# Kernel tuning notes

Hardware: AMD Instinct MI355X
Metric: run time of the kernel (lower is better)

The kernel has to match this reference:

```python
import jax, jax.numpy as jnp
import numpy as np

EPS = 1e-10       # module eps
COS_EPS = 1e-8    # torch F.cosine_similarity norm clamp
TAO = 0.0
LIP = 0.0
SQUARED = False
DETACH_HR = True
LAMB_LIP = 1
# p = 1.0 -> np.random.random() < p is always True, so the sampling mask is baked to True.


def setup_inputs() -> dict:
    key = jax.random.key(0)
    k1, k2, k3 = jax.random.split(key, 3)
    img = jax.random.normal(k1, (256, 4, 3, 112, 112), dtype=jnp.float32)
    feat = jax.random.normal(k2, (256, 4, 512), dtype=jnp.float32)
    feat_norm = jax.random.normal(k3, (256, 4, 1), dtype=jnp.float32)
    return {"img": img, "feat": feat, "feat_norm": feat_norm}


def reference(img, feat, feat_norm):
    # img: [B, K, C, H, W], feat: [B, K, D], feat_norm: [B, K, 1]
    fn0 = feat_norm[:, 0, 0]                                   # [B]
    cond = fn0 > -TAO                                          # [B] outer if per batch row
    w = jax.lax.stop_gradient(1.0 / (jnp.exp(fn0) + EPS))      # [B] adaptive weight (detached)

    # consecutive-frame image L2 distance (full-tensor sum per frame pair)
    img_diff = jnp.sqrt(jnp.sum((img[:, 1:] - img[:, :-1]) ** 2, axis=(2, 3, 4))) + EPS  # [B, K-1]
    # skip frames identical to frame 0 (torch.equal check)
    neq = jnp.any(img[:, 1:] != img[:, 0:1], axis=(2, 3, 4))   # [B, K-1]

    fa = feat[:, :-1]                                          # [B, K-1, D] (HR side of each pair)
    fb = feat[:, 1:]                                           # [B, K-1, D]
    if DETACH_HR:
        fa = jax.lax.stop_gradient(fa)
    na = jnp.maximum(jnp.linalg.norm(fa, axis=-1), COS_EPS)
    nb = jnp.maximum(jnp.linalg.norm(fb, axis=-1), COS_EPS)
    cos = jnp.sum(fa * fb, axis=-1) / (na * nb)                # [B, K-1]

    ratio = (1.0 - cos) / img_diff - LIP
    term = ratio ** 2 if SQUARED else jnp.maximum(ratio, 0.0)
    term = term * w[:, None]

    mask = cond[:, None] & neq
    penalty = jnp.sum(jnp.where(mask, term, 0.0), axis=1)      # [B]
    adaptive_weight_list = jnp.where(cond, w, 0.0)             # [B]
    return LAMB_LIP * jnp.mean(penalty), adaptive_weight_list
```

## Files before the change

### kernel.cpp

```cpp
#include <hip/hip_runtime.h>
#include <math.h>

#define EPS 1e-10f
#define COS_EPS 1e-8f

#define NB 256
#define NF 4
#define FRAME_F4 9408
#define BLK_PER_B 37
#define PART_STRIDE 64


__global__ __launch_bounds__(256) void img_stage(const float* __restrict__ img,
                                                 float* __restrict__ ws_sq_part,
                                                 int* __restrict__ ws_neq_part) {
    const int b   = blockIdx.y;
    const int bx  = blockIdx.x;
    const int tid = threadIdx.x;
    const int idx = bx * 256 + tid;

    float s1 = 0.f, s2 = 0.f, s3 = 0.f;
    int   n1 = 0,   n2 = 0,   n3 = 0;

    if (idx < FRAME_F4) {
        const float4* base = (const float4*)img + (size_t)b * NF * FRAME_F4;
        float4 f0 = base[idx];
        float4 f1 = base[FRAME_F4 + idx];
        float4 f2 = base[2 * FRAME_F4 + idx];
        float4 f3 = base[3 * FRAME_F4 + idx];

        float dx, dy, dz, dw;
        dx = f1.x - f0.x; dy = f1.y - f0.y; dz = f1.z - f0.z; dw = f1.w - f0.w;
        s1 = dx*dx + dy*dy + dz*dz + dw*dw;
        dx = f2.x - f1.x; dy = f2.y - f1.y; dz = f2.z - f1.z; dw = f2.w - f1.w;
        s2 = dx*dx + dy*dy + dz*dz + dw*dw;
        dx = f3.x - f2.x; dy = f3.y - f2.y; dz = f3.z - f2.z; dw = f3.w - f2.w;
        s3 = dx*dx + dy*dy + dz*dz + dw*dw;

        n1 = (f1.x != f0.x) | (f1.y != f0.y) | (f1.z != f0.z) | (f1.w != f0.w);
        n2 = (f2.x != f0.x) | (f2.y != f0.y) | (f2.z != f0.z) | (f2.w != f0.w);
        n3 = (f3.x != f0.x) | (f3.y != f0.y) | (f3.z != f0.z) | (f3.w != f0.w);
    }

    for (int off = 32; off > 0; off >>= 1) {
        s1 += __shfl_down(s1, off);
        s2 += __shfl_down(s2, off);
        s3 += __shfl_down(s3, off);
        n1 |= __shfl_down(n1, off);
        n2 |= __shfl_down(n2, off);
        n3 |= __shfl_down(n3, off);
    }

    __shared__ float ls[3][4];
    __shared__ int   ln[3][4];
    const int wave = tid >> 6;
    if ((tid & 63) == 0) {
        ls[0][wave] = s1; ls[1][wave] = s2; ls[2][wave] = s3;
        ln[0][wave] = n1; ln[1][wave] = n2; ln[2][wave] = n3;
    }
    __syncthreads();
    if (tid == 0) {
        const int base3 = b * 3;
        ws_sq_part[(base3 + 0) * PART_STRIDE + bx] = ls[0][0] + ls[0][1] + ls[0][2] + ls[0][3];
        ws_sq_part[(base3 + 1) * PART_STRIDE + bx] = ls[1][0] + ls[1][1] + ls[1][2] + ls[1][3];
        ws_sq_part[(base3 + 2) * PART_STRIDE + bx] = ls[2][0] + ls[2][1] + ls[2][2] + ls[2][3];
        ws_neq_part[(base3 + 0) * PART_STRIDE + bx] = ln[0][0] | ln[0][1] | ln[0][2] | ln[0][3];
        ws_neq_part[(base3 + 1) * PART_STRIDE + bx] = ln[1][0] | ln[1][1] | ln[1][2] | ln[1][3];
        ws_neq_part[(base3 + 2) * PART_STRIDE + bx] = ln[2][0] | ln[2][1] | ln[2][2] | ln[2][3];
    }
}

__global__ __launch_bounds__(192) void batch_stage(const float* __restrict__ feat,
                                                   const float* __restrict__ feat_norm,
                                                   const float* __restrict__ ws_sq_part,
                                                   const int* __restrict__ ws_neq_part,
                                                   float* __restrict__ out) {
    const int b    = blockIdx.x;
    const int tid  = threadIdx.x;
    const int p    = tid >> 6;
    const int lane = tid & 63;

    const float4* fa = (const float4*)feat + ((size_t)b * NF + p) * 128;
    const float4* fb = fa + 128;

    float dab = 0.f, daa = 0.f, dbb = 0.f;
#pragma unroll
    for (int j = 0; j < 2; ++j) {
        float4 a  = fa[lane + 64 * j];
        float4 bb = fb[lane + 64 * j];
        dab += a.x * bb.x + a.y * bb.y + a.z * bb.z + a.w * bb.w;
        daa += a.x * a.x + a.y * a.y + a.z * a.z + a.w * a.w;
        dbb += bb.x * bb.x + bb.y * bb.y + bb.z * bb.z + bb.w * bb.w;
    }

    const int slot = (b * 3 + p) * PART_STRIDE + lane;
    float sq = (lane < BLK_PER_B) ? ws_sq_part[slot] : 0.0f;
    int   nq = (lane < BLK_PER_B) ? ws_neq_part[slot] : 0;

    for (int off = 32; off > 0; off >>= 1) {
        dab += __shfl_down(dab, off);
        daa += __shfl_down(daa, off);
        dbb += __shfl_down(dbb, off);
        sq  += __shfl_down(sq, off);
        nq  |= __shfl_down(nq, off);
    }

    __shared__ float sh_term[3];
    if (lane == 0) {
        float na   = fmaxf(sqrtf(daa), COS_EPS);
        float nb   = fmaxf(sqrtf(dbb), COS_EPS);
        float cosv = dab / (na * nb);
        float img_diff = sqrtf(sq) + EPS;
        float ratio = (1.0f - cosv) / img_diff;
        float term  = fmaxf(ratio, 0.0f);
        float fn0   = feat_norm[b * NF];
        float w     = 1.0f / (expf(fn0) + EPS);
        bool  cond  = fn0 > 0.0f;
        sh_term[p]  = (cond && nq) ? term * w : 0.0f;
    }
    __syncthreads();
    if (tid == 0) {
        float fn0 = feat_norm[b * NF];
        float w   = 1.0f / (expf(fn0) + EPS);
        out[1 + b] = (fn0 > 0.0f) ? w : 0.0f;
        float pen = sh_term[0] + sh_term[1] + sh_term[2];
        atomicAdd(&out[0], pen * (1.0f / 256.0f));
    }
}

extern "C" void kernel_launch(void* const* d_in, const int* in_sizes, int n_in,
                              void* d_out, int out_size, void* d_ws, size_t ws_size,
                              hipStream_t stream) {
    const float* img       = (const float*)d_in[0];
    const float* feat      = (const float*)d_in[1];
    const float* feat_norm = (const float*)d_in[2];
    float* out = (float*)d_out;

    float* ws_sq_part = (float*)d_ws;
    int*   ws_neq_part = (int*)((char*)d_ws + 768 * PART_STRIDE * sizeof(float));

    hipMemsetAsync(out, 0, sizeof(float), stream);
    img_stage<<<dim3(BLK_PER_B, NB), 256, 0, stream>>>(img, ws_sq_part, ws_neq_part);
    batch_stage<<<NB, 192, 0, stream>>>(feat, feat_norm, ws_sq_part, ws_neq_part, out);
}
```

Measured before the change: 223.6 us.

## Fuse image and batch stages into one kernel with last-block-done reduction

Merges the two kernels into a single launch. Each image block atomically accumulates its partial sums and inequality flags per frame pair, and the last block to finish for a batch row, found through a per-row counter, computes the cosine term. A global counter lets the final block write the mean loss. This removes one kernel launch and the partial-array round trip, at the cost of atomics and thread fences, and makes the float summation order nondeterministic.

```diff
diff --git a/kernel.cpp b/kernel.cpp
--- a/kernel.cpp
+++ b/kernel.cpp
@@ -8,12 +8,17 @@
 #define NF 4
 #define FRAME_F4 9408
 #define BLK_PER_B 37
-#define PART_STRIDE 64
 
 
-__global__ __launch_bounds__(256) void img_stage(const float* __restrict__ img,
-                                                 float* __restrict__ ws_sq_part,
-                                                 int* __restrict__ ws_neq_part) {
+__global__ __launch_bounds__(256) void fused(const float* __restrict__ img,
+                                             const float* __restrict__ feat,
+                                             const float* __restrict__ feat_norm,
+                                             float* __restrict__ ws_sq,
+                                             int* __restrict__ ws_neq,
+                                             int* __restrict__ cnt,
+                                             int* __restrict__ cnt_g,
+                                             float* __restrict__ ws_loss,
+                                             float* __restrict__ out) {
     const int b   = blockIdx.y;
     const int bx  = blockIdx.x;
     const int tid = threadIdx.x;
@@ -53,6 +58,7 @@
 
     __shared__ float ls[3][4];
     __shared__ int   ln[3][4];
+    __shared__ bool  is_last;
     const int wave = tid >> 6;
     if ((tid & 63) == 0) {
         ls[0][wave] = s1; ls[1][wave] = s2; ls[2][wave] = s3;
@@ -61,62 +67,58 @@
     __syncthreads();
     if (tid == 0) {
         const int base3 = b * 3;
-        ws_sq_part[(base3 + 0) * PART_STRIDE + bx] = ls[0][0] + ls[0][1] + ls[0][2] + ls[0][3];
-        ws_sq_part[(base3 + 1) * PART_STRIDE + bx] = ls[1][0] + ls[1][1] + ls[1][2] + ls[1][3];
-        ws_sq_part[(base3 + 2) * PART_STRIDE + bx] = ls[2][0] + ls[2][1] + ls[2][2] + ls[2][3];
-        ws_neq_part[(base3 + 0) * PART_STRIDE + bx] = ln[0][0] | ln[0][1] | ln[0][2] | ln[0][3];
-        ws_neq_part[(base3 + 1) * PART_STRIDE + bx] = ln[1][0] | ln[1][1] | ln[1][2] | ln[1][3];
-        ws_neq_part[(base3 + 2) * PART_STRIDE + bx] = ln[2][0] | ln[2][1] | ln[2][2] | ln[2][3];
+        atomicAdd(&ws_sq[base3 + 0], ls[0][0] + ls[0][1] + ls[0][2] + ls[0][3]);
+        atomicAdd(&ws_sq[base3 + 1], ls[1][0] + ls[1][1] + ls[1][2] + ls[1][3]);
+        atomicAdd(&ws_sq[base3 + 2], ls[2][0] + ls[2][1] + ls[2][2] + ls[2][3]);
+        int m1 = ln[0][0] | ln[0][1] | ln[0][2] | ln[0][3];
+        int m2 = ln[1][0] | ln[1][1] | ln[1][2] | ln[1][3];
+        int m3 = ln[2][0] | ln[2][1] | ln[2][2] | ln[2][3];
+        if (m1) atomicOr(&ws_neq[base3 + 0], 1);
+        if (m2) atomicOr(&ws_neq[base3 + 1], 1);
+        if (m3) atomicOr(&ws_neq[base3 + 2], 1);
+        __threadfence();
+        int old = atomicAdd(&cnt[b], 1);
+        is_last = (old == BLK_PER_B - 1);
     }
-}
+    __syncthreads();
+    if (!is_last) return;
 
-__global__ __launch_bounds__(192) void batch_stage(const float* __restrict__ feat,
-                                                   const float* __restrict__ feat_norm,
-                                                   const float* __restrict__ ws_sq_part,
-                                                   const int* __restrict__ ws_neq_part,
-                                                   float* __restrict__ out) {
-    const int b    = blockIdx.x;
-    const int tid  = threadIdx.x;
     const int p    = tid >> 6;
     const int lane = tid & 63;
 
-    const float4* fa = (const float4*)feat + ((size_t)b * NF + p) * 128;
-    const float4* fb = fa + 128;
+    __shared__ float sh_term[3];
+    if (p < 3) {
+        const float4* fa = (const float4*)feat + ((size_t)b * NF + p) * 128;
+        const float4* fb = fa + 128;
 
-    float dab = 0.f, daa = 0.f, dbb = 0.f;
+        float dab = 0.f, daa = 0.f, dbb = 0.f;
 #pragma unroll
-    for (int j = 0; j < 2; ++j) {
-        float4 a  = fa[lane + 64 * j];
-        float4 bb = fb[lane + 64 * j];
-        dab += a.x * bb.x + a.y * bb.y + a.z * bb.z + a.w * bb.w;
-        daa += a.x * a.x + a.y * a.y + a.z * a.z + a.w * a.w;
-        dbb += bb.x * bb.x + bb.y * bb.y + bb.z * bb.z + bb.w * bb.w;
-    }
-
-    const int slot = (b * 3 + p) * PART_STRIDE + lane;
-    float sq = (lane < BLK_PER_B) ? ws_sq_part[slot] : 0.0f;
-    int   nq = (lane < BLK_PER_B) ? ws_neq_part[slot] : 0;
-
-    for (int off = 32; off > 0; off >>= 1) {
-        dab += __shfl_down(dab, off);
-        daa += __shfl_down(daa, off);
-        dbb += __shfl_down(dbb, off);
-        sq  += __shfl_down(sq, off);
-        nq  |= __shfl_down(nq, off);
-    }
-
-    __shared__ float sh_term[3];
-    if (lane == 0) {
-        float na   = fmaxf(sqrtf(daa), COS_EPS);
-        float nb   = fmaxf(sqrtf(dbb), COS_EPS);
-        float cosv = dab / (na * nb);
-        float img_diff = sqrtf(sq) + EPS;
-        float ratio = (1.0f - cosv) / img_diff;
-        float term  = fmaxf(ratio, 0.0f);
-        float fn0   = feat_norm[b * NF];
-        float w     = 1.0f / (expf(fn0) + EPS);
-        bool  cond  = fn0 > 0.0f;
-        sh_term[p]  = (cond && nq) ? term * w : 0.0f;
+        for (int j = 0; j < 2; ++j) {
+            float4 a  = fa[lane + 64 * j];
+            float4 bb = fb[lane + 64 * j];
+            dab += a.x * bb.x + a.y * bb.y + a.z * bb.z + a.w * bb.w;
+            daa += a.x * a.x + a.y * a.y + a.z * a.z + a.w * a.w;
+            dbb += bb.x * bb.x + bb.y * bb.y + bb.z * bb.z + bb.w * bb.w;
+        }
+        for (int off = 32; off > 0; off >>= 1) {
+            dab += __shfl_down(dab, off);
+            daa += __shfl_down(daa, off);
+            dbb += __shfl_down(dbb, off);
+        }
+        if (lane == 0) {
+            float sq = atomicAdd(&ws_sq[b * 3 + p], 0.0f);
+            int   nq = atomicOr(&ws_neq[b * 3 + p], 0);
+            float na   = fmaxf(sqrtf(daa), COS_EPS);
+            float nb   = fmaxf(sqrtf(dbb), COS_EPS);
+            float cosv = dab / (na * nb);
+            float img_diff = sqrtf(sq) + EPS;
+            float ratio = (1.0f - cosv) / img_diff;
+            float term  = fmaxf(ratio, 0.0f);
+            float fn0   = feat_norm[b * NF];
+            float w     = 1.0f / (expf(fn0) + EPS);
+            bool  cond  = fn0 > 0.0f;
+            sh_term[p]  = (cond && nq) ? term * w : 0.0f;
+        }
     }
     __syncthreads();
     if (tid == 0) {
@@ -124,7 +126,13 @@
         float w   = 1.0f / (expf(fn0) + EPS);
         out[1 + b] = (fn0 > 0.0f) ? w : 0.0f;
         float pen = sh_term[0] + sh_term[1] + sh_term[2];
-        atomicAdd(&out[0], pen * (1.0f / 256.0f));
+        atomicAdd(ws_loss, pen);
+        __threadfence();
+        int oldg = atomicAdd(cnt_g, 1);
+        if (oldg == NB - 1) {
+            float total = atomicAdd(ws_loss, 0.0f);
+            out[0] = total * (1.0f / 256.0f);
+        }
     }
 }
 
@@ -136,10 +144,15 @@
     const float* feat_norm = (const float*)d_in[2];
     float* out = (float*)d_out;
 
-    float* ws_sq_part = (float*)d_ws;
-    int*   ws_neq_part = (int*)((char*)d_ws + 768 * PART_STRIDE * sizeof(float));
+    char* ws = (char*)d_ws;
+    float* ws_sq   = (float*)ws;
+    int*   ws_neq  = (int*)(ws + 768 * 4);
+    int*   cnt     = (int*)(ws + 1536 * 4);
+    int*   cnt_g   = (int*)(ws + 1792 * 4);
+    float* ws_loss = (float*)(ws + 1793 * 4);
 
-    hipMemsetAsync(out, 0, sizeof(float), stream);
-    img_stage<<<dim3(BLK_PER_B, NB), 256, 0, stream>>>(img, ws_sq_part, ws_neq_part);
-    batch_stage<<<NB, 192, 0, stream>>>(feat, feat_norm, ws_sq_part, ws_neq_part, out);
+    hipMemsetAsync(d_ws, 0, 1794 * 4, stream);
+    fused<<<dim3(BLK_PER_B, NB), 256, 0, stream>>>(img, feat, feat_norm,
+                                                   ws_sq, ws_neq, cnt, cnt_g,
+                                                   ws_loss, out);
 }
```

New measurement: 654.6 us. 2.93x slower.

## Fuse image-diff and feature-cosine stages into one per-batch kernel

Applied to the files above, without the earlier changes.

Merges the two kernels into one launch where each 1024-thread block handles a whole batch row. The block loops over the frame pixels, reduces the pair sums in shared memory and then computes the cosine term directly, so the workspace round trip and the second launch go away. The cost is a grid of only 256 blocks streaming about 600KB each, which may underuse the 256 CUs' memory bandwidth compared with the earlier 37x256-block grid.

```diff
diff --git a/kernel.cpp b/kernel.cpp
--- a/kernel.cpp
+++ b/kernel.cpp
@@ -7,23 +7,20 @@
 #define NB 256
 #define NF 4
 #define FRAME_F4 9408
-#define BLK_PER_B 37
-#define PART_STRIDE 64
 
+__global__ __launch_bounds__(1024) void fused(const float* __restrict__ img,
+                                              const float* __restrict__ feat,
+                                              const float* __restrict__ feat_norm,
+                                              float* __restrict__ out) {
+    const int b   = blockIdx.x;
+    const int tid = threadIdx.x;
 
-__global__ __launch_bounds__(256) void img_stage(const float* __restrict__ img,
-                                                 float* __restrict__ ws_sq_part,
-                                                 int* __restrict__ ws_neq_part) {
-    const int b   = blockIdx.y;
-    const int bx  = blockIdx.x;
-    const int tid = threadIdx.x;
-    const int idx = bx * 256 + tid;
+    const float4* base = (const float4*)img + (size_t)b * NF * FRAME_F4;
 
     float s1 = 0.f, s2 = 0.f, s3 = 0.f;
     int   n1 = 0,   n2 = 0,   n3 = 0;
 
-    if (idx < FRAME_F4) {
-        const float4* base = (const float4*)img + (size_t)b * NF * FRAME_F4;
+    for (int idx = tid; idx < FRAME_F4; idx += 1024) {
         float4 f0 = base[idx];
         float4 f1 = base[FRAME_F4 + idx];
         float4 f2 = base[2 * FRAME_F4 + idx];
@@ -31,15 +28,15 @@
 
         float dx, dy, dz, dw;
         dx = f1.x - f0.x; dy = f1.y - f0.y; dz = f1.z - f0.z; dw = f1.w - f0.w;
-        s1 = dx*dx + dy*dy + dz*dz + dw*dw;
+        s1 += dx*dx + dy*dy + dz*dz + dw*dw;
         dx = f2.x - f1.x; dy = f2.y - f1.y; dz = f2.z - f1.z; dw = f2.w - f1.w;
-        s2 = dx*dx + dy*dy + dz*dz + dw*dw;
+        s2 += dx*dx + dy*dy + dz*dz + dw*dw;
         dx = f3.x - f2.x; dy = f3.y - f2.y; dz = f3.z - f2.z; dw = f3.w - f2.w;
-        s3 = dx*dx + dy*dy + dz*dz + dw*dw;
+        s3 += dx*dx + dy*dy + dz*dz + dw*dw;
 
-        n1 = (f1.x != f0.x) | (f1.y != f0.y) | (f1.z != f0.z) | (f1.w != f0.w);
-        n2 = (f2.x != f0.x) | (f2.y != f0.y) | (f2.z != f0.z) | (f2.w != f0.w);
-        n3 = (f3.x != f0.x) | (f3.y != f0.y) | (f3.z != f0.z) | (f3.w != f0.w);
+        n1 |= (f1.x != f0.x) | (f1.y != f0.y) | (f1.z != f0.z) | (f1.w != f0.w);
+        n2 |= (f2.x != f0.x) | (f2.y != f0.y) | (f2.z != f0.z) | (f2.w != f0.w);
+        n3 |= (f3.x != f0.x) | (f3.y != f0.y) | (f3.z != f0.z) | (f3.w != f0.w);
     }
 
     for (int off = 32; off > 0; off >>= 1) {
@@ -51,72 +48,54 @@
         n3 |= __shfl_down(n3, off);
     }
 
-    __shared__ float ls[3][4];
-    __shared__ int   ln[3][4];
+    __shared__ float ls[3][16];
+    __shared__ int   ln[3][16];
     const int wave = tid >> 6;
-    if ((tid & 63) == 0) {
+    const int lane = tid & 63;
+    if (lane == 0) {
         ls[0][wave] = s1; ls[1][wave] = s2; ls[2][wave] = s3;
         ln[0][wave] = n1; ln[1][wave] = n2; ln[2][wave] = n3;
     }
     __syncthreads();
-    if (tid == 0) {
-        const int base3 = b * 3;
-        ws_sq_part[(base3 + 0) * PART_STRIDE + bx] = ls[0][0] + ls[0][1] + ls[0][2] + ls[0][3];
-        ws_sq_part[(base3 + 1) * PART_STRIDE + bx] = ls[1][0] + ls[1][1] + ls[1][2] + ls[1][3];
-        ws_sq_part[(base3 + 2) * PART_STRIDE + bx] = ls[2][0] + ls[2][1] + ls[2][2] + ls[2][3];
-        ws_neq_part[(base3 + 0) * PART_STRIDE + bx] = ln[0][0] | ln[0][1] | ln[0][2] | ln[0][3];
-        ws_neq_part[(base3 + 1) * PART_STRIDE + bx] = ln[1][0] | ln[1][1] | ln[1][2] | ln[1][3];
-        ws_neq_part[(base3 + 2) * PART_STRIDE + bx] = ln[2][0] | ln[2][1] | ln[2][2] | ln[2][3];
-    }
-}
 
-__global__ __launch_bounds__(192) void batch_stage(const float* __restrict__ feat,
-                                                   const float* __restrict__ feat_norm,
-                                                   const float* __restrict__ ws_sq_part,
-                                                   const int* __restrict__ ws_neq_part,
-                                                   float* __restrict__ out) {
-    const int b    = blockIdx.x;
-    const int tid  = threadIdx.x;
-    const int p    = tid >> 6;
-    const int lane = tid & 63;
+    const int p = wave;
+    __shared__ float sh_term[3];
+    if (p < 3) {
+        float sq = (lane < 16) ? ls[p][lane] : 0.0f;
+        int   nq = (lane < 16) ? ln[p][lane] : 0;
 
-    const float4* fa = (const float4*)feat + ((size_t)b * NF + p) * 128;
-    const float4* fb = fa + 128;
+        const float4* fa = (const float4*)feat + ((size_t)b * NF + p) * 128;
+        const float4* fb = fa + 128;
 
-    float dab = 0.f, daa = 0.f, dbb = 0.f;
+        float dab = 0.f, daa = 0.f, dbb = 0.f;
 #pragma unroll
-    for (int j = 0; j < 2; ++j) {
-        float4 a  = fa[lane + 64 * j];
-        float4 bb = fb[lane + 64 * j];
-        dab += a.x * bb.x + a.y * bb.y + a.z * bb.z + a.w * bb.w;
-        daa += a.x * a.x + a.y * a.y + a.z * a.z + a.w * a.w;
-        dbb += bb.x * bb.x + bb.y * bb.y + bb.z * bb.z + bb.w * bb.w;
-    }
+        for (int j = 0; j < 2; ++j) {
+            float4 a  = fa[lane + 64 * j];
+            float4 bb = fb[lane + 64 * j];
+            dab += a.x * bb.x + a.y * bb.y + a.z * bb.z + a.w * bb.w;
+            daa += a.x * a.x + a.y * a.y + a.z * a.z + a.w * a.w;
+            dbb += bb.x * bb.x + bb.y * bb.y + bb.z * bb.z + bb.w * bb.w;
+        }
+        for (int off = 32; off > 0; off >>= 1) {
+            dab += __shfl_down(dab, off);
+            daa += __shfl_down(daa, off);
+            dbb += __shfl_down(dbb, off);
+            sq  += __shfl_down(sq, off);
+            nq  |= __shfl_down(nq, off);
+        }
 
-    const int slot = (b * 3 + p) * PART_STRIDE + lane;
-    float sq = (lane < BLK_PER_B) ? ws_sq_part[slot] : 0.0f;
-    int   nq = (lane < BLK_PER_B) ? ws_neq_part[slot] : 0;
-
-    for (int off = 32; off > 0; off >>= 1) {
-        dab += __shfl_down(dab, off);
-        daa += __shfl_down(daa, off);
-        dbb += __shfl_down(dbb, off);
-        sq  += __shfl_down(sq, off);
-        nq  |= __shfl_down(nq, off);
-    }
-
-    __shared__ float sh_term[3];
-    if (lane == 0) {
-        float na   = fmaxf(sqrtf(daa), COS_EPS);
-        float nb   = fmaxf(sqrtf(dbb), COS_EPS);
-        float cosv = dab / (na * nb);
-        float img_diff = sqrtf(sq) + EPS;
-        float ratio = (1.0f - cosv) / img_diff;
-        float term  = fmaxf(ratio, 0.0f);
-        float fn0   = feat_norm[b * NF];
-        float w     = 1.0f / (expf(fn0) + EPS);
-        bool  cond  = fn0 > 0.0f;
-        sh_term[p]  = (cond && nq) ? term * w : 0.0f;
+        if (lane == 0) {
+            float na   = fmaxf(sqrtf(daa), COS_EPS);
+            float nb   = fmaxf(sqrtf(dbb), COS_EPS);
+            float cosv = dab / (na * nb);
+            float img_diff = sqrtf(sq) + EPS;
+            float ratio = (1.0f - cosv) / img_diff;
+            float term  = fmaxf(ratio, 0.0f);
+            float fn0   = feat_norm[b * NF];
+            float w     = 1.0f / (expf(fn0) + EPS);
+            bool  cond  = fn0 > 0.0f;
+            sh_term[p]  = (cond && nq) ? term * w : 0.0f;
+        }
     }
     __syncthreads();
     if (tid == 0) {
@@ -136,10 +115,6 @@
     const float* feat_norm = (const float*)d_in[2];
     float* out = (float*)d_out;
 
-    float* ws_sq_part = (float*)d_ws;
-    int*   ws_neq_part = (int*)((char*)d_ws + 768 * PART_STRIDE * sizeof(float));
-
     hipMemsetAsync(out, 0, sizeof(float), stream);
-    img_stage<<<dim3(BLK_PER_B, NB), 256, 0, stream>>>(img, ws_sq_part, ws_neq_part);
-    batch_stage<<<NB, 192, 0, stream>>>(feat, feat_norm, ws_sq_part, ws_neq_part, out);
+    fused<<<NB, 1024, 0, stream>>>(img, feat, feat_norm, out);
 }
```

Result: no change. 221.8 us (-0.8%).
